# Kernel optimization log

Measured on AMD Instinct MI355X. Metric: run time of the kernel, lower is better.

## Reference

```python
import jax, jax.numpy as jnp
import numpy as np

N_NODES = 100000
N_EDGES = 1200000
D_IN = 64
D_OUT = 32
BN_EPS = 1e-5


def setup_inputs() -> dict:
    key = jax.random.key(0)
    ks = jax.random.split(key, 8)
    x = jax.random.normal(ks[0], (N_NODES, D_IN), dtype=jnp.float32)
    edge_index = jax.random.randint(ks[1], (2, N_EDGES), 0, N_NODES, dtype=jnp.int64)
    W1s = jax.random.normal(ks[2], (3, D_IN, D_IN), dtype=jnp.float32) * 0.05
    b1s = jax.random.normal(ks[3], (3, D_IN), dtype=jnp.float32) * 0.05
    W2s = jax.random.normal(ks[4], (3, D_IN, D_IN), dtype=jnp.float32) * 0.05
    b2s = jax.random.normal(ks[5], (3, D_IN), dtype=jnp.float32) * 0.05
    gammas = jnp.ones((3, D_IN), dtype=jnp.float32)
    betas = jnp.zeros((3, D_IN), dtype=jnp.float32)
    epss = jnp.zeros((3,), dtype=jnp.float32)  # GINConv train_eps init value 0
    lin_w = jax.random.normal(ks[6], (D_IN, D_OUT), dtype=jnp.float32) * 0.05
    lin_b = jnp.zeros((D_OUT,), dtype=jnp.float32)
    return {"x": x, "edge_index": edge_index, "W1s": W1s, "b1s": b1s,
            "W2s": W2s, "b2s": b2s, "gammas": gammas, "betas": betas,
            "epss": epss, "lin_w": lin_w, "lin_b": lin_b}


def reference(x, edge_index, W1s, b1s, W2s, b2s, gammas, betas, epss, lin_w, lin_b):
    # PyG GINConv (source_to_target): out_i = nn((1+eps)*x_i + sum_{j->i} x_j)
    src = edge_index[0]
    dst = edge_index[1]
    n = x.shape[0]
    h = x
    for i in range(3):
        agg = jax.ops.segment_sum(h[src], dst, num_segments=n)  # [N, d]
        z = (1.0 + epss[i]) * h + agg
        z = jax.nn.relu(z @ W1s[i] + b1s[i])
        z = jax.nn.relu(z @ W2s[i] + b2s[i])
        # BatchNorm1d, training mode (batch statistics, biased variance)
        mu = jnp.mean(z, axis=0)
        var = jnp.var(z, axis=0)
        z = gammas[i] * (z - mu) * jax.lax.rsqrt(var + BN_EPS) + betas[i]
        h = jax.nn.relu(z)  # F.relu after each conv
    return h @ lin_w + lin_b  # [N, D_OUT]
```

## Files before the change

kernel.cpp:

```cpp
#include <hip/hip_runtime.h>
#include <hip/hip_fp16.h>

#define NBMAX 256
#define BCAP  8192
#define CHB   3584

typedef _Float16 half8 __attribute__((ext_vector_type(8)));
typedef float f32x4 __attribute__((ext_vector_type(4)));

__device__ __forceinline__ unsigned short f2h(float f) {
    __half h = __float2half_rn(f);
    return *(unsigned short*)&h;
}

__device__ __forceinline__ int scan256(int v, int* wsum, int* woff) {
    int t = threadIdx.x, lane = t & 63, wv = t >> 6;
    int x = v;
    #pragma unroll
    for (int d = 1; d < 64; d <<= 1) {
        int y = __shfl_up(x, d, 64);
        if (lane >= d) x += y;
    }
    if (lane == 63) wsum[wv] = x;
    __syncthreads();
    if (t == 0) {
        int a = 0;
        #pragma unroll
        for (int i = 0; i < 4; ++i) { woff[i] = a; a += wsum[i]; }
    }
    __syncthreads();
    return x - v + woff[wv];
}

__global__ __launch_bounds__(256) void gin_x16init(const float* __restrict__ x,
                                                   unsigned short* __restrict__ o, int n16,
                                                   const void* __restrict__ edge,
                                                   int* __restrict__ flag,
                                                   int* __restrict__ gcount, int nb,
                                                   float* __restrict__ stats, int E) {
    if (blockIdx.x == gridDim.x - 1) {
        int t = threadIdx.x;
        for (int i = t; i < nb; i += 256) gcount[i] = 0;
        for (int i = t; i < 384; i += 256) stats[i] = 0.f;
        if (t == 0) {
            const int* p = (const int*)edge;
            int is64 = 1;
            int m = (E < 64) ? E : 64;
            for (int i = 0; i < m; ++i)
                if (p[2 * i + 1] != 0) is64 = 0;
            *flag = is64;
        }
        return;
    }
    int i = blockIdx.x * 256 + threadIdx.x;
    if (i >= n16) return;
    float4 v = ((const float4*)x)[i];
    ushort4 u;
    u.x = f2h(v.x); u.y = f2h(v.y); u.z = f2h(v.z); u.w = f2h(v.w);
    ((ushort4*)o)[i] = u;
}

__global__ __launch_bounds__(256) void gin_binscatter(const void* __restrict__ edge,
                                                      const int* __restrict__ flag,
                                                      int* __restrict__ gcount,
                                                      uint2* __restrict__ ebuf, int E, int nb) {
    __shared__ int cnt[NBMAX];
    __shared__ int dlt[NBMAX];
    __shared__ int cur[NBMAX];
    __shared__ int wsum[4], woff[4];
    __shared__ uint2 buf[CHB];
    int t = threadIdx.x;
    int beg = blockIdx.x * CHB;
    int m = E - beg; if (m > CHB) m = CHB;
    if (t < nb) cnt[t] = 0;
    __syncthreads();
    int is64 = *flag;
    for (int j = t; j < m; j += 256) {
        int e = beg + j;
        int d = is64 ? (int)((const long long*)edge)[E + e] : ((const int*)edge)[E + e];
        atomicAdd(&cnt[d >> 9], 1);
    }
    __syncthreads();
    int v = (t < nb) ? cnt[t] : 0;
    int excl = scan256(v, wsum, woff);
    if (t < nb) {
        int gb = v ? atomicAdd(&gcount[t], v) : 0;
        dlt[t] = t * BCAP + gb - excl;
        cur[t] = excl;
    }
    __syncthreads();
    for (int j = t; j < m; j += 256) {
        int e = beg + j;
        int s, d;
        if (is64) {
            s = (int)((const long long*)edge)[e];
            d = (int)((const long long*)edge)[E + e];
        } else {
            s = ((const int*)edge)[e];
            d = ((const int*)edge)[E + e];
        }
        int p = atomicAdd(&cur[d >> 9], 1);
        buf[p] = make_uint2((unsigned)s, (unsigned)d);
    }
    __syncthreads();
    for (int j = t; j < m; j += 256) {
        uint2 ed = buf[j];
        ebuf[j + dlt[(int)(ed.y >> 9)]] = ed;
    }
}

__global__ __launch_bounds__(256) void gin_build(const uint2* __restrict__ ebuf,
                                                 const int* __restrict__ gcount,
                                                 int* __restrict__ rowbeg,
                                                 int* __restrict__ rowend,
                                                 int* __restrict__ col, int n) {
    __shared__ int cnt[512];
    __shared__ int off[512];
    __shared__ int wsum[4], woff[4];
    int b = blockIdx.x, t = threadIdx.x;
    int beg = b * BCAP;
    int end = beg + gcount[b];
    cnt[t] = 0; cnt[t + 256] = 0;
    __syncthreads();
    for (int j = beg + t; j < end; j += 256)
        atomicAdd(&cnt[(int)(ebuf[j].y & 511)], 1);
    __syncthreads();
    int v0 = cnt[2 * t], v1 = cnt[2 * t + 1];
    int ep = scan256(v0 + v1, wsum, woff);
    off[2 * t] = ep;
    off[2 * t + 1] = ep + v0;
    __syncthreads();
    int node0 = b * 512 + 2 * t;
    if (node0 < n) {
        rowbeg[node0] = beg + off[2 * t];
        rowend[node0] = beg + off[2 * t] + v0;
    }
    if (node0 + 1 < n) {
        rowbeg[node0 + 1] = beg + off[2 * t + 1];
        rowend[node0 + 1] = beg + off[2 * t + 1] + v1;
    }
    __syncthreads();
    for (int j = beg + t; j < end; j += 256) {
        uint2 ed = ebuf[j];
        int p = atomicAdd(&off[(int)(ed.y & 511)], 1);
        col[beg + p] = (int)ed.x;
    }
}

template <bool APPLY>
__device__ __forceinline__ void accum8(float* acc, uint4 u,
                                       const float* sc, const float* sh) {
    float v[8];
    float2 f;
    f = __half22float2(*(const __half2*)&u.x); v[0] = f.x; v[1] = f.y;
    f = __half22float2(*(const __half2*)&u.y); v[2] = f.x; v[3] = f.y;
    f = __half22float2(*(const __half2*)&u.z); v[4] = f.x; v[5] = f.y;
    f = __half22float2(*(const __half2*)&u.w); v[6] = f.x; v[7] = f.y;
    #pragma unroll
    for (int j = 0; j < 8; ++j)
        acc[j] += APPLY ? fmaxf(fmaf(v[j], sc[j], sh[j]), 0.f) : v[j];
}

template <bool APPLY>
__device__ __forceinline__ void gather_node(const unsigned short* __restrict__ zb,
                                            int r0, int r1, int ci0,
                                            const int* __restrict__ col,
                                            float e1,
                                            const float* sc, const float* sh,
                                            _Float16* __restrict__ trow,
                                            int wid, int qn, int l16) {
    int r = l16 >> 3, c = l16 & 7;
    uint4 su = make_uint4(0, 0, 0, 0);
    if (r == 0) su = *(const uint4*)(zb + (size_t)wid * 64 + 8 * c);

    float acc[8] = {0.f, 0.f, 0.f, 0.f, 0.f, 0.f, 0.f, 0.f};
    int ci = ci0;
    for (int b2 = r0; b2 < r1; b2 += 16) {
        if (b2 > r0) {
            int ce = b2 + l16;
            ci = col[ce < r1 ? ce : r1 - 1];
        }
        uint4 u[8];
        bool p[8];
        #pragma unroll
        for (int s = 0; s < 8; ++s) {
            int j = 2 * s + r;
            p[s] = (b2 + j) < r1;
            int idx = __shfl(ci, 16 * qn + j);
            if (p[s]) u[s] = *(const uint4*)(zb + (size_t)idx * 64 + 8 * c);
        }
        #pragma unroll
        for (int s = 0; s < 8; ++s)
            if (p[s]) accum8<APPLY>(acc, u[s], sc, sh);
    }
    #pragma unroll
    for (int j = 0; j < 8; ++j)
        acc[j] += __shfl_xor(acc[j], 8);
    if (r == 0) {
        float s[8];
        float2 f;
        f = __half22float2(*(const __half2*)&su.x); s[0] = f.x; s[1] = f.y;
        f = __half22float2(*(const __half2*)&su.y); s[2] = f.x; s[3] = f.y;
        f = __half22float2(*(const __half2*)&su.z); s[4] = f.x; s[5] = f.y;
        f = __half22float2(*(const __half2*)&su.w); s[6] = f.x; s[7] = f.y;
        #pragma unroll
        for (int j = 0; j < 8; ++j) {
            float v = APPLY ? fmaxf(fmaf(s[j], sc[j], sh[j]), 0.f) : s[j];
            acc[j] = fmaf(e1, v, acc[j]);
        }
        uint4 o;
        o.x = (unsigned)f2h(acc[0]) | ((unsigned)f2h(acc[1]) << 16);
        o.y = (unsigned)f2h(acc[2]) | ((unsigned)f2h(acc[3]) << 16);
        o.z = (unsigned)f2h(acc[4]) | ((unsigned)f2h(acc[5]) << 16);
        o.w = (unsigned)f2h(acc[6]) | ((unsigned)f2h(acc[7]) << 16);
        *(uint4*)(trow + 8 * c) = o;
    }
}

template <bool APPLY>
__global__ __launch_bounds__(512, 4) void gin_fused(const unsigned short* __restrict__ zb,
                                                    const int* __restrict__ rowbeg,
                                                    const int* __restrict__ rowend,
                                                    const int* __restrict__ col,
                                                    const float* __restrict__ epss,
                                                    const float* __restrict__ gammas,
                                                    const float* __restrict__ betas,
                                                    float fN,
                                                    unsigned short* __restrict__ z16,
                                                    const float* __restrict__ W1g,
                                                    const float* __restrict__ b1g,
                                                    const float* __restrict__ W2g,
                                                    const float* __restrict__ b2g,
                                                    float* __restrict__ stats,
                                                    int layer, int n) {
    __shared__ _Float16 Wt[2 * 64 * 72];
    __shared__ _Float16 Tz[128 * 72];
    __shared__ float sS[64], sQ[64];
    __shared__ float sBN[128];
    int tid = threadIdx.x;
    int base = blockIdx.x * 128;
    const float* __restrict__ W1 = W1g + layer * 4096;
    const float* __restrict__ W2 = W2g + layer * 4096;

    for (int i = tid; i < 4096; i += 512) {
        int k = i >> 6, nn = i & 63;
        Wt[nn * 72 + k]        = (_Float16)W1[i];
        Wt[4608 + nn * 72 + k] = (_Float16)W2[i];
    }
    if (tid < 64) {
        sS[tid] = 0.f; sQ[tid] = 0.f;
        if (APPLY) {
            float mu  = stats[(layer - 1) * 128 + tid] / fN;
            float var = stats[(layer - 1) * 128 + 64 + tid] / fN - mu * mu;
            float g   = gammas[(layer - 1) * 64 + tid];
            float grs = g * rsqrtf(var + 1e-5f);
            sBN[tid]      = grs;
            sBN[64 + tid] = betas[(layer - 1) * 64 + tid] - grs * mu;
        }
    }
    __syncthreads();

    int lane = tid & 63, wv = tid >> 6;
    int qn = lane >> 4;
    int l16 = lane & 15;
    int c8 = l16 & 7;
    float e1 = 1.f + epss[layer];
    float sc[8] = {1.f, 1.f, 1.f, 1.f, 1.f, 1.f, 1.f, 1.f};
    float sh[8] = {0.f, 0.f, 0.f, 0.f, 0.f, 0.f, 0.f, 0.f};
    if (APPLY) {
        *(float4*)&sc[0] = *(const float4*)&sBN[8 * c8];
        *(float4*)&sc[4] = *(const float4*)&sBN[8 * c8 + 4];
        *(float4*)&sh[0] = *(const float4*)&sBN[64 + 8 * c8];
        *(float4*)&sh[4] = *(const float4*)&sBN[64 + 8 * c8 + 4];
    }

    int wvq = wv * 4 + qn;
    int cr0, cr1, pr0, pr1;
    {
        int w0 = base + wvq;
        cr0 = 0; cr1 = 0;
        if (w0 < n) { cr0 = rowbeg[w0]; cr1 = rowend[w0]; }
        int w1 = w0 + 32;
        pr0 = 0; pr1 = 0;
        if (w1 < n) { pr0 = rowbeg[w1]; pr1 = rowend[w1]; }
    }
    int cci = 0;
    if (cr1 > cr0) { int ce = cr0 + l16; cci = col[ce < cr1 ? ce : cr1 - 1]; }
    #pragma unroll 1
    for (int p = 0; p < 4; ++p) {
        int nci = 0;
        if (pr1 > pr0) { int ce = pr0 + l16; nci = col[ce < pr1 ? ce : pr1 - 1]; }
        int fr0 = 0, fr1 = 0;
        {
            int w2 = base + (p + 2) * 32 + wvq;
            if (p < 2 && w2 < n) { fr0 = rowbeg[w2]; fr1 = rowend[w2]; }
        }
        int widl = p * 32 + wvq;
        int wid = base + widl;
        if (wid < n) {
            gather_node<APPLY>(zb, cr0, cr1, cci, col, e1, sc, sh,
                               Tz + widl * 72, wid, qn, l16);
        } else if (l16 < 8) {
            *(uint4*)(Tz + widl * 72 + 8 * c8) = make_uint4(0u, 0u, 0u, 0u);
        }
        cr0 = pr0; cr1 = pr1; cci = nci;
        pr0 = fr0; pr1 = fr1;
    }
    __syncthreads();

    int g = qn, q = l16;
    int n0 = 16 * wv + q;

    half8 tb0 = *(const half8*)&Tz[n0 * 72 + 8 * g];
    half8 tb1 = *(const half8*)&Tz[n0 * 72 + 32 + 8 * g];

    f32x4 acc[4];
    #pragma unroll
    for (int ft = 0; ft < 4; ++ft)
        acc[ft] = (f32x4){0.f, 0.f, 0.f, 0.f};

    #pragma unroll
    for (int ft = 0; ft < 4; ++ft) {
        half8 a0 = *(const half8*)&Wt[(16 * ft + q) * 72 + 8 * g];
        half8 a1 = *(const half8*)&Wt[(16 * ft + q) * 72 + 32 + 8 * g];
        acc[ft] = __builtin_amdgcn_mfma_f32_16x16x32_f16(a0, tb0, acc[ft], 0, 0, 0);
        acc[ft] = __builtin_amdgcn_mfma_f32_16x16x32_f16(a1, tb1, acc[ft], 0, 0, 0);
    }

    #pragma unroll
    for (int ft = 0; ft < 4; ++ft) {
        float4 b = *(const float4*)(b1g + layer * 64 + 16 * ft + 4 * g);
        float v0 = fmaxf(acc[ft][0] + b.x, 0.f);
        float v1 = fmaxf(acc[ft][1] + b.y, 0.f);
        float v2 = fmaxf(acc[ft][2] + b.z, 0.f);
        float v3 = fmaxf(acc[ft][3] + b.w, 0.f);
        uint2 pk;
        pk.x = (unsigned)f2h(v0) | ((unsigned)f2h(v1) << 16);
        pk.y = (unsigned)f2h(v2) | ((unsigned)f2h(v3) << 16);
        *(uint2*)&Tz[n0 * 72 + 16 * ft + 4 * g] = pk;
    }

    half8 zb0 = *(const half8*)&Tz[n0 * 72 + 8 * g];
    half8 zb1 = *(const half8*)&Tz[n0 * 72 + 32 + 8 * g];
    #pragma unroll
    for (int ft = 0; ft < 4; ++ft)
        acc[ft] = (f32x4){0.f, 0.f, 0.f, 0.f};
    #pragma unroll
    for (int ft = 0; ft < 4; ++ft) {
        half8 a0 = *(const half8*)&Wt[4608 + (16 * ft + q) * 72 + 8 * g];
        half8 a1 = *(const half8*)&Wt[4608 + (16 * ft + q) * 72 + 32 + 8 * g];
        acc[ft] = __builtin_amdgcn_mfma_f32_16x16x32_f16(a0, zb0, acc[ft], 0, 0, 0);
        acc[ft] = __builtin_amdgcn_mfma_f32_16x16x32_f16(a1, zb1, acc[ft], 0, 0, 0);
    }

    int nodeg = base + n0;
    #pragma unroll
    for (int ft = 0; ft < 4; ++ft) {
        float4 b = *(const float4*)(b2g + layer * 64 + 16 * ft + 4 * g);
        float v0 = fmaxf(acc[ft][0] + b.x, 0.f);
        float v1 = fmaxf(acc[ft][1] + b.y, 0.f);
        float v2 = fmaxf(acc[ft][2] + b.z, 0.f);
        float v3 = fmaxf(acc[ft][3] + b.w, 0.f);
        float s[4], sq[4];
        bool ok = nodeg < n;
        s[0] = ok ? v0 : 0.f; sq[0] = ok ? v0 * v0 : 0.f;
        s[1] = ok ? v1 : 0.f; sq[1] = ok ? v1 * v1 : 0.f;
        s[2] = ok ? v2 : 0.f; sq[2] = ok ? v2 * v2 : 0.f;
        s[3] = ok ? v3 : 0.f; sq[3] = ok ? v3 * v3 : 0.f;
        uint2 pk;
        pk.x = (unsigned)f2h(v0) | ((unsigned)f2h(v1) << 16);
        pk.y = (unsigned)f2h(v2) | ((unsigned)f2h(v3) << 16);
        *(uint2*)&Tz[n0 * 72 + 16 * ft + 4 * g] = pk;
        #pragma unroll
        for (int off = 1; off < 16; off <<= 1) {
            #pragma unroll
            for (int r2 = 0; r2 < 4; ++r2) {
                s[r2] += __shfl_xor(s[r2], off);
                sq[r2] += __shfl_xor(sq[r2], off);
            }
        }
        if (q == 0) {
            #pragma unroll
            for (int r2 = 0; r2 < 4; ++r2) {
                atomicAdd(&sS[16 * ft + 4 * g + r2], s[r2]);
                atomicAdd(&sQ[16 * ft + 4 * g + r2], sq[r2]);
            }
        }
    }

    #pragma unroll
    for (int t2 = 0; t2 < 2; ++t2) {
        int u = lane + 64 * t2;
        int rloc = 16 * wv + (u >> 3);
        int node = base + rloc;
        if (node < n) {
            uint4 v = *(const uint4*)&Tz[rloc * 72 + (u & 7) * 8];
            *(uint4*)(z16 + (size_t)node * 64 + (u & 7) * 8) = v;
        }
    }

    __syncthreads();
    if (tid < 64) {
        atomicAdd(&stats[layer * 128 + tid], sS[tid]);
        atomicAdd(&stats[layer * 128 + 64 + tid], sQ[tid]);
    }
}

__global__ __launch_bounds__(256) void gin_lin(const unsigned short* __restrict__ zin,
                                               const float* __restrict__ stats,
                                               const float* __restrict__ gammas,
                                               const float* __restrict__ betas,
                                               float fN,
                                               const float* __restrict__ lw,
                                               const float* __restrict__ lb,
                                               float* __restrict__ out, int n) {
    __shared__ float Z[128 * 68];
    int tid = threadIdx.x;
    int base = blockIdx.x * 128;
    int cq = (tid & 15) * 4;
    float4 sc4, sh4;
    {
        float t0[4], t1[4];
        #pragma unroll
        for (int j = 0; j < 4; ++j) {
            int f = cq + j;
            float mu  = stats[256 + f] / fN;
            float var = stats[256 + 64 + f] / fN - mu * mu;
            float g   = gammas[128 + f];
            float grs = g * rsqrtf(var + 1e-5f);
            t0[j] = grs;
            t1[j] = betas[128 + f] - grs * mu;
        }
        sc4 = make_float4(t0[0], t0[1], t0[2], t0[3]);
        sh4 = make_float4(t1[0], t1[1], t1[2], t1[3]);
    }
    {
        const ushort4* __restrict__ src = (const ushort4*)(zin + (size_t)base * 64);
        #pragma unroll
        for (int it = 0; it < 8; ++it) {
            int idx4 = it * 256 + tid;
            int row = idx4 >> 4, c = (idx4 & 15) * 4;
            float4 v = make_float4(0.f, 0.f, 0.f, 0.f);
            if (base + row < n) {
                ushort4 u = src[idx4];
                float2 f0 = __half22float2(*(const __half2*)&u.x);
                float2 f1 = __half22float2(*(const __half2*)&u.z);
                v = make_float4(f0.x, f0.y, f1.x, f1.y);
            }
            float4 r;
            r.x = fmaxf(fmaf(v.x, sc4.x, sh4.x), 0.f);
            r.y = fmaxf(fmaf(v.y, sc4.y, sh4.y), 0.f);
            r.z = fmaxf(fmaf(v.z, sc4.z, sh4.z), 0.f);
            r.w = fmaxf(fmaf(v.w, sc4.w, sh4.w), 0.f);
            *(float4*)&Z[row * 68 + c] = r;
        }
    }
    __syncthreads();
    int tx = tid & 7, ty = tid >> 3;
    float acc[4][4];
    {
        float4 b = *(const float4*)(lb + 4 * tx);
        #pragma unroll
        for (int r = 0; r < 4; ++r) {
            acc[r][0] = b.x; acc[r][1] = b.y; acc[r][2] = b.z; acc[r][3] = b.w;
        }
    }
    #pragma unroll 4
    for (int k = 0; k < 64; ++k) {
        float4 w = *(const float4*)(lw + k * 32 + 4 * tx);
        #pragma unroll
        for (int r = 0; r < 4; ++r) {
            float a = Z[(ty + 32 * r) * 68 + k];
            acc[r][0] = fmaf(a, w.x, acc[r][0]);
            acc[r][1] = fmaf(a, w.y, acc[r][1]);
            acc[r][2] = fmaf(a, w.z, acc[r][2]);
            acc[r][3] = fmaf(a, w.w, acc[r][3]);
        }
    }
    #pragma unroll
    for (int r = 0; r < 4; ++r) {
        int row = base + ty + 32 * r;
        if (row < n) {
            float4 v;
            v.x = acc[r][0]; v.y = acc[r][1]; v.z = acc[r][2]; v.w = acc[r][3];
            *(float4*)(out + (size_t)row * 32 + 4 * tx) = v;
        }
    }
}

extern "C" void kernel_launch(void* const* d_in, const int* in_sizes, int n_in,
                              void* d_out, int out_size, void* d_ws, size_t ws_size,
                              hipStream_t stream) {
    const float* x      = (const float*)d_in[0];
    const void*  edge   = d_in[1];
    const float* W1s    = (const float*)d_in[2];
    const float* b1s    = (const float*)d_in[3];
    const float* W2s    = (const float*)d_in[4];
    const float* b2s    = (const float*)d_in[5];
    const float* gammas = (const float*)d_in[6];
    const float* betas  = (const float*)d_in[7];
    const float* epss   = (const float*)d_in[8];
    const float* lin_w  = (const float*)d_in[9];
    const float* lin_b  = (const float*)d_in[10];
    float* out = (float*)d_out;

    const int N = in_sizes[0] / 64;
    const int E = in_sizes[1] / 2;
    const int NB = (N + 511) >> 9;
    const float fN = (float)N;

    char* w = (char*)d_ws;
    auto take = [&](size_t bytes) {
        char* p = w;
        w += (bytes + 255) & ~(size_t)255;
        return p;
    };
    unsigned short* x16 = (unsigned short*)take((size_t)N * 64 * 2);
    unsigned short* hA  = (unsigned short*)take((size_t)N * 64 * 2);
    unsigned short* hB  = (unsigned short*)take((size_t)N * 64 * 2);
    uint2* ebuf    = (uint2*)take((size_t)NB * BCAP * 8);
    int*   col     = (int*)take((size_t)NB * BCAP * 4);
    int*   rowbeg  = (int*)take((size_t)N * 4);
    int*   rowend  = (int*)take((size_t)N * 4);
    int*   gcount  = (int*)take((size_t)NBMAX * 4);
    float* stats   = (float*)take(3 * 128 * 4);
    int*   flag    = (int*)take(4);

    const int n16 = N * 16;
    gin_x16init<<<(n16 + 255) / 256 + 1, 256, 0, stream>>>(x, x16, n16, edge, flag,
                                                           gcount, NB, stats, E);
    gin_binscatter<<<(E + CHB - 1) / CHB, 256, 0, stream>>>(edge, flag, gcount, ebuf, E, NB);
    gin_build<<<NB, 256, 0, stream>>>(ebuf, gcount, rowbeg, rowend, col, N);

    const int gMlp = (N + 127) / 128;
    const unsigned short* zin = x16;
    unsigned short* zout = hA;
    for (int L = 0; L < 3; ++L) {
        if (L == 0)
            gin_fused<false><<<gMlp, 512, 0, stream>>>(zin, rowbeg, rowend, col, epss,
                                                       gammas, betas, fN, zout,
                                                       W1s, b1s, W2s, b2s, stats, L, N);
        else
            gin_fused<true><<<gMlp, 512, 0, stream>>>(zin, rowbeg, rowend, col, epss,
                                                      gammas, betas, fN, zout,
                                                      W1s, b1s, W2s, b2s, stats, L, N);
        zin = zout;
        zout = (zout == hA) ? hB : hA;
    }
    gin_lin<<<gMlp, 256, 0, stream>>>(zin, stats, gammas, betas, fN, lin_w, lin_b, out, N);
}
```

Before: 309.4 us.

## Split fp16 node features into two 32-feature halves for cache-friendly gathers

Stores the fp16 node feature matrix as two planar halves (features 0-31 and 32-63), each with a 64-byte row stride. The gather loop now runs twice per node group, one pass per half, with 4 lanes per row and 4 neighbours per iteration, and reduces partial sums over two shuffle levels. The aim is to make each random-gather pass touch a half-size working set (3.2MB per half) that fits better in L2/MALL. The cost is doubled index traversal and loop overhead, plus strided access in the conversion, writeback and final linear kernels.

Result: slower. 346.8 us (+12.1%).

```diff
diff --git a/kernel.cpp b/kernel.cpp
--- a/kernel.cpp
+++ b/kernel.cpp
@@ -54,10 +54,13 @@
     }
     int i = blockIdx.x * 256 + threadIdx.x;
     if (i >= n16) return;
+    int nn = n16 >> 4;
     float4 v = ((const float4*)x)[i];
     ushort4 u;
     u.x = f2h(v.x); u.y = f2h(v.y); u.z = f2h(v.z); u.w = f2h(v.w);
-    ((ushort4*)o)[i] = u;
+    int node = i >> 4, g = i & 15;
+    int h = g >> 3, gi = g & 7;
+    ((ushort4*)o)[(size_t)h * ((size_t)nn * 8) + (size_t)node * 8 + gi] = u;
 }
 
 __global__ __launch_bounds__(256) void gin_binscatter(const void* __restrict__ edge,
@@ -162,16 +165,16 @@
 }
 
 template <bool APPLY>
-__device__ __forceinline__ void gather_node(const unsigned short* __restrict__ zb,
+__device__ __forceinline__ void gather_half(const unsigned short* __restrict__ zh,
                                             int r0, int r1, int ci0,
                                             const int* __restrict__ col,
                                             float e1,
                                             const float* sc, const float* sh,
                                             _Float16* __restrict__ trow,
                                             int wid, int qn, int l16) {
-    int r = l16 >> 3, c = l16 & 7;
+    int r = l16 >> 2, c = l16 & 3;
     uint4 su = make_uint4(0, 0, 0, 0);
-    if (r == 0) su = *(const uint4*)(zb + (size_t)wid * 64 + 8 * c);
+    if (r == 0) su = *(const uint4*)(zh + (size_t)wid * 32 + 8 * c);
 
     float acc[8] = {0.f, 0.f, 0.f, 0.f, 0.f, 0.f, 0.f, 0.f};
     int ci = ci0;
@@ -180,22 +183,24 @@
             int ce = b2 + l16;
             ci = col[ce < r1 ? ce : r1 - 1];
         }
-        uint4 u[8];
-        bool p[8];
-        #pragma unroll
-        for (int s = 0; s < 8; ++s) {
-            int j = 2 * s + r;
+        uint4 u[4];
+        bool p[4];
+        #pragma unroll
+        for (int s = 0; s < 4; ++s) {
+            int j = 4 * s + r;
             p[s] = (b2 + j) < r1;
             int idx = __shfl(ci, 16 * qn + j);
-            if (p[s]) u[s] = *(const uint4*)(zb + (size_t)idx * 64 + 8 * c);
-        }
-        #pragma unroll
-        for (int s = 0; s < 8; ++s)
+            if (p[s]) u[s] = *(const uint4*)(zh + (size_t)idx * 32 + 8 * c);
+        }
+        #pragma unroll
+        for (int s = 0; s < 4; ++s)
             if (p[s]) accum8<APPLY>(acc, u[s], sc, sh);
     }
     #pragma unroll
-    for (int j = 0; j < 8; ++j)
+    for (int j = 0; j < 8; ++j) {
+        acc[j] += __shfl_xor(acc[j], 4);
         acc[j] += __shfl_xor(acc[j], 8);
+    }
     if (r == 0) {
         float s[8];
         float2 f;
@@ -263,16 +268,9 @@
     int lane = tid & 63, wv = tid >> 6;
     int qn = lane >> 4;
     int l16 = lane & 15;
-    int c8 = l16 & 7;
+    int c4 = l16 & 3;
     float e1 = 1.f + epss[layer];
-    float sc[8] = {1.f, 1.f, 1.f, 1.f, 1.f, 1.f, 1.f, 1.f};
-    float sh[8] = {0.f, 0.f, 0.f, 0.f, 0.f, 0.f, 0.f, 0.f};
-    if (APPLY) {
-        *(float4*)&sc[0] = *(const float4*)&sBN[8 * c8];
-        *(float4*)&sc[4] = *(const float4*)&sBN[8 * c8 + 4];
-        *(float4*)&sh[0] = *(const float4*)&sBN[64 + 8 * c8];
-        *(float4*)&sh[4] = *(const float4*)&sBN[64 + 8 * c8 + 4];
-    }
+    const size_t hstride = (size_t)n * 32;
 
     int wvq = wv * 4 + qn;
     int cr0, cr1, pr0, pr1;
@@ -280,28 +278,40 @@
         int w0 = base + wvq;
         cr0 = 0; cr1 = 0;
         if (w0 < n) { cr0 = rowbeg[w0]; cr1 = rowend[w0]; }
-        int w1 = w0 + 32;
+        int w1 = base + 32 + wvq;
         pr0 = 0; pr1 = 0;
         if (w1 < n) { pr0 = rowbeg[w1]; pr1 = rowend[w1]; }
     }
     int cci = 0;
     if (cr1 > cr0) { int ce = cr0 + l16; cci = col[ce < cr1 ? ce : cr1 - 1]; }
+    float sc[8] = {1.f, 1.f, 1.f, 1.f, 1.f, 1.f, 1.f, 1.f};
+    float sh[8] = {0.f, 0.f, 0.f, 0.f, 0.f, 0.f, 0.f, 0.f};
     #pragma unroll 1
-    for (int p = 0; p < 4; ++p) {
+    for (int j = 0; j < 8; ++j) {
+        int h = j >> 2, p = j & 3;
         int nci = 0;
         if (pr1 > pr0) { int ce = pr0 + l16; nci = col[ce < pr1 ? ce : pr1 - 1]; }
         int fr0 = 0, fr1 = 0;
-        {
-            int w2 = base + (p + 2) * 32 + wvq;
-            if (p < 2 && w2 < n) { fr0 = rowbeg[w2]; fr1 = rowend[w2]; }
+        if (j < 6) {
+            int w2 = base + ((j + 2) & 3) * 32 + wvq;
+            if (w2 < n) { fr0 = rowbeg[w2]; fr1 = rowend[w2]; }
+        }
+        if (APPLY) {
+            const float* pS = &sBN[32 * h + 8 * c4];
+            *(float4*)&sc[0] = *(const float4*)pS;
+            *(float4*)&sc[4] = *(const float4*)(pS + 4);
+            *(float4*)&sh[0] = *(const float4*)(pS + 64);
+            *(float4*)&sh[4] = *(const float4*)(pS + 68);
         }
         int widl = p * 32 + wvq;
         int wid = base + widl;
+        const unsigned short* zh = zb + (size_t)h * hstride;
+        _Float16* trow = Tz + widl * 72 + 32 * h;
         if (wid < n) {
-            gather_node<APPLY>(zb, cr0, cr1, cci, col, e1, sc, sh,
-                               Tz + widl * 72, wid, qn, l16);
-        } else if (l16 < 8) {
-            *(uint4*)(Tz + widl * 72 + 8 * c8) = make_uint4(0u, 0u, 0u, 0u);
+            gather_half<APPLY>(zh, cr0, cr1, cci, col, e1, sc, sh,
+                               trow, wid, qn, l16);
+        } else if (l16 < 4) {
+            *(uint4*)(trow + 8 * l16) = make_uint4(0u, 0u, 0u, 0u);
         }
         cr0 = pr0; cr1 = pr1; cci = nci;
         pr0 = fr0; pr1 = fr1;
@@ -389,13 +399,13 @@
     }
 
     #pragma unroll
-    for (int t2 = 0; t2 < 2; ++t2) {
-        int u = lane + 64 * t2;
-        int rloc = 16 * wv + (u >> 3);
+    for (int h2 = 0; h2 < 2; ++h2) {
+        int rloc = 16 * wv + (lane >> 2);
+        int cp = lane & 3;
         int node = base + rloc;
         if (node < n) {
-            uint4 v = *(const uint4*)&Tz[rloc * 72 + (u & 7) * 8];
-            *(uint4*)(z16 + (size_t)node * 64 + (u & 7) * 8) = v;
+            uint4 v = *(const uint4*)&Tz[rloc * 72 + 32 * h2 + 8 * cp];
+            *(uint4*)(z16 + (size_t)h2 * hstride + (size_t)node * 32 + 8 * cp) = v;
         }
     }
 
@@ -435,14 +445,17 @@
         sh4 = make_float4(t1[0], t1[1], t1[2], t1[3]);
     }
     {
-        const ushort4* __restrict__ src = (const ushort4*)(zin + (size_t)base * 64);
+        const size_t hstride = (size_t)n * 32;
         #pragma unroll
         for (int it = 0; it < 8; ++it) {
             int idx4 = it * 256 + tid;
-            int row = idx4 >> 4, c = (idx4 & 15) * 4;
+            int row = idx4 >> 4, cfeat = (idx4 & 15) * 4;
+            int h = cfeat >> 5, cin = cfeat & 31;
             float4 v = make_float4(0.f, 0.f, 0.f, 0.f);
             if (base + row < n) {
-                ushort4 u = src[idx4];
+                const unsigned short* zp = zin + (size_t)h * hstride
+                                         + (size_t)(base + row) * 32 + cin;
+                ushort4 u = *(const ushort4*)zp;
                 float2 f0 = __half22float2(*(const __half2*)&u.x);
                 float2 f1 = __half22float2(*(const __half2*)&u.z);
                 v = make_float4(f0.x, f0.y, f1.x, f1.y);
@@ -452,7 +465,7 @@
             r.y = fmaxf(fmaf(v.y, sc4.y, sh4.y), 0.f);
             r.z = fmaxf(fmaf(v.z, sc4.z, sh4.z), 0.f);
             r.w = fmaxf(fmaf(v.w, sc4.w, sh4.w), 0.f);
-            *(float4*)&Z[row * 68 + c] = r;
+            *(float4*)&Z[row * 68 + cfeat] = r;
         }
     }
     __syncthreads();
```
